# Performance work log

Hardware: AMD Instinct MI355X
Metric: run time of the kernel (lower is better)

The kernel has to match this reference:

```python
import jax, jax.numpy as jnp
import numpy as np

NEG_INF = -1e30
EPS = 1e-6


def _apply_rope_interleaved(x, cos, sin):
    # x: (..., rope_dim); cos/sin broadcastable to (..., rope_dim//2)
    x1 = x[..., 0::2]
    x2 = x[..., 1::2]
    o1 = x1 * cos - x2 * sin
    o2 = x1 * sin + x2 * cos
    return jnp.stack([o1, o2], axis=-1).reshape(x.shape)


def setup_inputs() -> dict:
    key = jax.random.key(0)
    ks = jax.random.split(key, 6)
    B, S, D = 1, 2048, 7168
    H, HD, ROPE, QLR = 64, 128, 64, 1536
    x = jax.random.normal(ks[0], (B, S, D), dtype=jnp.float32)
    q_lora = jax.random.normal(ks[1], (B, S, QLR), dtype=jnp.float32)
    wq_b = jax.random.normal(ks[2], (QLR, H * HD), dtype=jnp.float32) * 0.02
    wk = jax.random.normal(ks[3], (D, HD), dtype=jnp.float32) * 0.02
    weights_proj = jax.random.normal(ks[4], (D, H), dtype=jnp.float32) * 0.02
    k_norm_w = jnp.ones((HD,), dtype=jnp.float32)
    k_norm_b = jnp.zeros((HD,), dtype=jnp.float32)
    # standard RoPE tables for the first ROPE dims
    half = ROPE // 2
    inv_freq = 1.0 / (10000.0 ** (np.arange(half, dtype=np.float64) / half))
    ang = np.arange(S, dtype=np.float64)[:, None] * inv_freq[None, :]
    cos = jnp.asarray(np.cos(ang), dtype=jnp.float32)
    sin = jnp.asarray(np.sin(ang), dtype=jnp.float32)
    return {"x": x, "q_lora": q_lora, "wq_b": wq_b, "wk": wk,
            "weights_proj": weights_proj, "k_norm_w": k_norm_w,
            "k_norm_b": k_norm_b, "cos": cos, "sin": sin, "topk": 512}


def reference(x, q_lora, wq_b, wk, weights_proj, k_norm_w, k_norm_b, cos, sin, topk):
    B, S, D = x.shape
    HD = wk.shape[1]
    H = weights_proj.shape[1]
    ROPE = cos.shape[1] * 2
    # queries: low-rank up-projection -> per-head, RoPE on first ROPE dims
    q = (q_lora @ wq_b).reshape(B, S, H, HD)
    q_pe = _apply_rope_interleaved(q[..., :ROPE], cos[None, :, None, :], sin[None, :, None, :])
    q = jnp.concatenate([q_pe, q[..., ROPE:]], axis=-1)
    # keys: single head, LayerNorm then RoPE on first ROPE dims
    k = x @ wk  # [B,S,HD]
    mu = k.mean(-1, keepdims=True)
    var = ((k - mu) ** 2).mean(-1, keepdims=True)
    k = (k - mu) * jax.lax.rsqrt(var + EPS) * k_norm_w + k_norm_b
    k_pe = _apply_rope_interleaved(k[..., :ROPE], cos[None], sin[None])
    k = jnp.concatenate([k_pe, k[..., ROPE:]], axis=-1)
    # per-token head gates, scaled by n_heads^-0.5 and softmax scale HD^-0.5
    w = (x @ weights_proj) * (H ** -0.5) * (HD ** -0.5)  # [B,S,H]
    # lightning index score: I[t,s] = sum_h w[t,h] * relu(q[t,h] . k[s])
    scores = jax.nn.relu(jnp.einsum('bshd,btd->bsht', q, k))  # [B,S,H,S]
    index_score = jnp.einsum('bsht,bsh->bst', scores, w)      # [B,S,S]
    # causal mask then top-k token selection
    causal = jnp.arange(S)[None, :] <= jnp.arange(S)[:, None]
    index_score = jnp.where(causal[None], index_score, NEG_INF)
    vals, idx = jax.lax.top_k(index_score, topk)
    return vals, idx
```

## Files before the change

### kernel.cpp

```cpp
#include <hip/hip_runtime.h>
#include <stdint.h>

#define S_LEN 2048
#define D_DIM 7168
#define H_NUM 64
#define HD_DIM 128
#define QLR_DIM 1536
#define NQ_DIM 8192
#define ROPE_DIM 64
#define HALF_DIM 32
#define TOPK_N 512
#define NEG_INF_F (-1e30f)
#define LN_EPS 1e-6f
#define W_SCALE 0.011048543456039806f

#define KCHUNKS 7
#define KCHUNK_SZ 1024

#define QF_HSTRIDE (128 * 4 * 64 * 8)

#define QBF_OFF 0
#define ALORA_OFF (QBF_OFF + S_LEN * NQ_DIM / 2)
#define WT_OFF   (ALORA_OFF + S_LEN * QLR_DIM / 2)
#define XBF_OFF  (WT_OFF + NQ_DIM * QLR_DIM / 2)
#define WT2_OFF  (XBF_OFF + S_LEN * D_DIM / 2)
#define KF_OFF   (WT2_OFF + 192 * D_DIM / 2)
#define KBF_OFF  (KF_OFF + S_LEN * HD_DIM)
#define WF_OFF   (KBF_OFF + S_LEN * HD_DIM / 2)
#define SC_OFF   (WF_OFF + S_LEN * H_NUM)

typedef __attribute__((ext_vector_type(8))) short short8;
typedef __attribute__((ext_vector_type(4))) float floatx4;

__device__ __forceinline__ ushort f2bf(float f) {
    unsigned int u = __float_as_uint(f);
    u += 0x7FFFu + ((u >> 16) & 1u);
    return (ushort)(u >> 16);
}
__device__ __forceinline__ unsigned int pack2bf(float lo, float hi) {
    return (unsigned int)f2bf(lo) | ((unsigned int)f2bf(hi) << 16);
}

__device__ __forceinline__ void gld_lds16(const ushort* g, ushort* l) {
    __builtin_amdgcn_global_load_lds(
        (const __attribute__((address_space(1))) unsigned int*)g,
        (__attribute__((address_space(3))) unsigned int*)l, 16, 0, 0);
}

__global__ __launch_bounds__(256) void cast_bf16_kernel(
    const float* __restrict__ in, ushort* __restrict__ out)
{
    int g = (blockIdx.x * 256 + threadIdx.x) * 8;
    float4 a = *(const float4*)&in[g];
    float4 b = *(const float4*)&in[g + 4];
    uint4 v;
    v.x = pack2bf(a.x, a.y); v.y = pack2bf(a.z, a.w);
    v.z = pack2bf(b.x, b.y); v.w = pack2bf(b.z, b.w);
    *(uint4*)&out[g] = v;
}

__global__ __launch_bounds__(256) void transpose_wqb_kernel(
    const float* __restrict__ W, ushort* __restrict__ WT)
{
    __shared__ ushort tl[64][72];
    const int n0 = blockIdx.x * 64, k0 = blockIdx.y * 64;
    const int t = threadIdx.x;
    const int r = t >> 4, c4 = (t & 15) * 4;
#pragma unroll
    for (int u = 0; u < 4; u++) {
        int kk = r + u * 16;
        float4 v = *(const float4*)&W[(size_t)(k0 + kk) * NQ_DIM + n0 + c4];
        tl[c4 + 0][kk] = f2bf(v.x);
        tl[c4 + 1][kk] = f2bf(v.y);
        tl[c4 + 2][kk] = f2bf(v.z);
        tl[c4 + 3][kk] = f2bf(v.w);
    }
    __syncthreads();
#pragma unroll
    for (int u = 0; u < 2; u++) {
        int i = t + u * 256;
        int nr = i >> 3, c8 = (i & 7) * 8;
        uint4 v = *(const uint4*)&tl[nr][c8];
        *(uint4*)&WT[(size_t)(n0 + nr) * QLR_DIM + k0 + c8] = v;
    }
}

__global__ __launch_bounds__(256) void transpose_wkp_kernel(
    const float* __restrict__ WK, const float* __restrict__ WP,
    ushort* __restrict__ WT2)
{
    __shared__ ushort tl[64][72];
    const int ntile = blockIdx.x;
    const int k0 = blockIdx.y * 64;
    const float* src; int ld, cbase;
    if (ntile < 2) { src = WK; ld = HD_DIM; cbase = ntile * 64; }
    else           { src = WP; ld = H_NUM; cbase = 0; }
    const int t = threadIdx.x;
    const int r = t >> 4, c4 = (t & 15) * 4;
#pragma unroll
    for (int u = 0; u < 4; u++) {
        int kk = r + u * 16;
        float4 v = *(const float4*)&src[(size_t)(k0 + kk) * ld + cbase + c4];
        tl[c4 + 0][kk] = f2bf(v.x);
        tl[c4 + 1][kk] = f2bf(v.y);
        tl[c4 + 2][kk] = f2bf(v.z);
        tl[c4 + 3][kk] = f2bf(v.w);
    }
    __syncthreads();
#pragma unroll
    for (int u = 0; u < 2; u++) {
        int i = t + u * 256;
        int nr = i >> 3, c8 = (i & 7) * 8;
        uint4 v = *(const uint4*)&tl[nr][c8];
        *(uint4*)&WT2[(size_t)(ntile * 64 + nr) * D_DIM + k0 + c8] = v;
    }
}

__global__ __launch_bounds__(256) void qgemm_mfma_kernel(
    const ushort* __restrict__ Abf,
    const ushort* __restrict__ WT,
    const float* __restrict__ cosp, const float* __restrict__ sinp,
    ushort* __restrict__ Qo)
{
    __shared__ ushort lds[128 * 136];
    ushort* As = lds;
    ushort* Bs = lds + 8192;

    const int tid = threadIdx.x;
    const int lane = tid & 63;
    const int wave = tid >> 6;
    const int m = lane & 15;
    const int q = lane >> 4;
    const int wm = wave & 1, wn = wave >> 1;
    const int m0 = blockIdx.y * 128;
    const int n0 = blockIdx.x * 128;
    const int h = blockIdx.x;

    floatx4 acc[4][4];
#pragma unroll
    for (int i = 0; i < 4; i++)
#pragma unroll
        for (int j = 0; j < 4; j++) acc[i][j] = (floatx4){0.f, 0.f, 0.f, 0.f};

    const ushort* agp[4];
    const ushort* bgp[4];
    unsigned int sbase[4];
#pragma unroll
    for (int u = 0; u < 4; u++) {
        int s = (u * 4 + wave) * 64 + lane;
        int row = s >> 3, c = s & 7;
        int kg = c ^ (row & 7);
        agp[u] = Abf + (size_t)(m0 + row) * QLR_DIM + kg * 8;
        bgp[u] = WT + (size_t)(n0 + row) * QLR_DIM + kg * 8;
        sbase[u] = (unsigned int)((u * 4 + wave) * 64 * 8);
    }

    for (int kt = 0; kt < QLR_DIM; kt += 64) {
        __syncthreads();
#pragma unroll
        for (int u = 0; u < 4; u++) gld_lds16(agp[u] + kt, &As[sbase[u]]);
#pragma unroll
        for (int u = 0; u < 4; u++) gld_lds16(bgp[u] + kt, &Bs[sbase[u]]);
        __syncthreads();

        short8 af[4][2], bf[4][2];
#pragma unroll
        for (int mt = 0; mt < 4; mt++) {
            int row = wm * 64 + mt * 16 + m;
#pragma unroll
            for (int ks = 0; ks < 2; ks++)
                af[mt][ks] = *(const short8*)
                    &As[row * 64 + ((((ks << 2) + q) ^ (m & 7)) * 8)];
        }
#pragma unroll
        for (int nt = 0; nt < 4; nt++) {
            int row = wn * 64 + nt * 16 + m;
#pragma unroll
            for (int ks = 0; ks < 2; ks++)
                bf[nt][ks] = *(const short8*)
                    &Bs[row * 64 + ((((ks << 2) + q) ^ (m & 7)) * 8)];
        }
#pragma unroll
        for (int mt = 0; mt < 4; mt++)
#pragma unroll
            for (int nt = 0; nt < 4; nt++)
#pragma unroll
                for (int ks = 0; ks < 2; ks++)
                    acc[mt][nt] = __builtin_amdgcn_mfma_f32_16x16x32_bf16(
                        af[mt][ks], bf[nt][ks], acc[mt][nt], 0, 0, 0);
    }

    __syncthreads();
    ushort* ep = lds;

#pragma unroll
    for (int mt = 0; mt < 4; mt++) {
        const int srow_base = m0 + wm * 64 + mt * 16 + q * 4;
#pragma unroll
        for (int nt = 0; nt < 4; nt++) {
            const int d = wn * 64 + nt * 16 + m;
            float o[4];
            if (wn == 0) {
                const int jj = d >> 1;
#pragma unroll
                for (int r = 0; r < 4; r++) {
                    float x = acc[mt][nt][r];
                    float p = __shfl_xor(x, 1, 64);
                    float c = cosp[(srow_base + r) * HALF_DIM + jj];
                    float sn = sinp[(srow_base + r) * HALF_DIM + jj];
                    o[r] = (d & 1) ? (p * sn + x * c) : (x * c - p * sn);
                }
            } else {
#pragma unroll
                for (int r = 0; r < 4; r++) o[r] = acc[mt][nt][r];
            }
#pragma unroll
            for (int r = 0; r < 4; r++)
                ep[(wm * 64 + mt * 16 + q * 4 + r) * 136 + d] = f2bf(o[r]);
        }
    }
    __syncthreads();

    const int sgrp0 = m0 >> 4;
#pragma unroll
    for (int u = 0; u < 8; u++) {
        int i = u * 256 + tid;
        int sgl = i >> 8, c = i & 255;
        int ks = c >> 6, ln = c & 63;
        int srow = sgl * 16 + (ln & 15);
        int d0 = (ks << 5) + ((ln >> 4) << 3);
        uint4 v = *(const uint4*)&ep[srow * 136 + d0];
        size_t dst = (size_t)h * QF_HSTRIDE +
                     ((((size_t)(sgrp0 + sgl) * 4 + ks) * 64 + ln) * 8);
        *(uint4*)&Qo[dst] = v;
    }
}

__global__ __launch_bounds__(256) void kw_mfma_kernel(
    const ushort* __restrict__ Xbf,
    const ushort* __restrict__ WT2,
    float* __restrict__ partial)
{
    __shared__ ushort As[128 * 64];
    __shared__ ushort Bs[64 * 64];

    const int tid = threadIdx.x;
    const int lane = tid & 63;
    const int wave = tid >> 6;
    const int m = lane & 15;
    const int q = lane >> 4;
    const int wm = wave & 1, wn = wave >> 1;
    const int m0 = blockIdx.x * 128;
    const int n0 = blockIdx.y * 64;
    const int kc = blockIdx.z;
    const size_t kbase = (size_t)kc * KCHUNK_SZ;

    const ushort* agp[4];
    unsigned int abase[4];
#pragma unroll
    for (int u = 0; u < 4; u++) {
        int s = (u * 4 + wave) * 64 + lane;
        int row = s >> 3, c = s & 7;
        int kg = c ^ (row & 7);
        agp[u] = Xbf + (size_t)(m0 + row) * D_DIM + kbase + kg * 8;
        abase[u] = (unsigned int)((u * 4 + wave) * 64 * 8);
    }
    const ushort* bgp[2];
    unsigned int bbase[2];
#pragma unroll
    for (int u = 0; u < 2; u++) {
        int s = (u * 4 + wave) * 64 + lane;
        int row = s >> 3, c = s & 7;
        int kg = c ^ (row & 7);
        bgp[u] = WT2 + (size_t)(n0 + row) * D_DIM + kbase + kg * 8;
        bbase[u] = (unsigned int)((u * 4 + wave) * 64 * 8);
    }

    floatx4 acc[4][2];
#pragma unroll
    for (int i = 0; i < 4; i++)
#pragma unroll
        for (int j = 0; j < 2; j++) acc[i][j] = (floatx4){0.f, 0.f, 0.f, 0.f};

    for (int kt = 0; kt < KCHUNK_SZ; kt += 64) {
        __syncthreads();
#pragma unroll
        for (int u = 0; u < 4; u++) gld_lds16(agp[u] + kt, &As[abase[u]]);
#pragma unroll
        for (int u = 0; u < 2; u++) gld_lds16(bgp[u] + kt, &Bs[bbase[u]]);
        __syncthreads();

        short8 af[4][2], bfr[2][2];
#pragma unroll
        for (int mt = 0; mt < 4; mt++) {
            int row = wm * 64 + mt * 16 + m;
#pragma unroll
            for (int ks = 0; ks < 2; ks++)
                af[mt][ks] = *(const short8*)
                    &As[row * 64 + ((((ks << 2) + q) ^ (m & 7)) * 8)];
        }
#pragma unroll
        for (int nt = 0; nt < 2; nt++) {
            int row = wn * 32 + nt * 16 + m;
#pragma unroll
            for (int ks = 0; ks < 2; ks++)
                bfr[nt][ks] = *(const short8*)
                    &Bs[row * 64 + ((((ks << 2) + q) ^ (m & 7)) * 8)];
        }
#pragma unroll
        for (int mt = 0; mt < 4; mt++)
#pragma unroll
            for (int nt = 0; nt < 2; nt++)
#pragma unroll
                for (int ks = 0; ks < 2; ks++)
                    acc[mt][nt] = __builtin_amdgcn_mfma_f32_16x16x32_bf16(
                        af[mt][ks], bfr[nt][ks], acc[mt][nt], 0, 0, 0);
    }

#pragma unroll
    for (int mt = 0; mt < 4; mt++) {
        int grow = m0 + wm * 64 + mt * 16 + q * 4;
#pragma unroll
        for (int nt = 0; nt < 2; nt++) {
            int gn = n0 + wn * 32 + nt * 16 + m;
#pragma unroll
            for (int r = 0; r < 4; r++)
                partial[((size_t)kc * S_LEN + grow + r) * 192 + gn] = acc[mt][nt][r];
        }
    }
}

__global__ __launch_bounds__(256) void kw_reduce_kernel(
    const float* __restrict__ partial, float* __restrict__ Ko, float* __restrict__ Wo)
{
    int g = blockIdx.x * 256 + threadIdx.x;
    int m = g / 192, n = g % 192;
    float s = 0.f;
#pragma unroll
    for (int c = 0; c < KCHUNKS; c++)
        s += partial[((size_t)c * S_LEN + m) * 192 + n];
    if (n < HD_DIM) Ko[(size_t)m * HD_DIM + n] = s;
    else            Wo[(size_t)m * H_NUM + (n - HD_DIM)] = s * W_SCALE;
}

__global__ __launch_bounds__(128) void knorm_rope_kernel(
    const float* __restrict__ Kf, const float* __restrict__ gw, const float* __restrict__ gb,
    const float* __restrict__ cosp, const float* __restrict__ sinp,
    ushort* __restrict__ Kbf)
{
    __shared__ float red[128];
    __shared__ float sh[128];
    const int m = blockIdx.x, t = threadIdx.x;
    float v = Kf[(size_t)m * HD_DIM + t];
    red[t] = v; __syncthreads();
    for (int off = 64; off > 0; off >>= 1) {
        if (t < off) red[t] += red[t + off];
        __syncthreads();
    }
    float mu = red[0] * (1.f / HD_DIM);
    __syncthreads();
    float dv = v - mu;
    red[t] = dv * dv; __syncthreads();
    for (int off = 64; off > 0; off >>= 1) {
        if (t < off) red[t] += red[t + off];
        __syncthreads();
    }
    float var = red[0] * (1.f / HD_DIM);
    float rs = rsqrtf(var + LN_EPS);
    float kn = dv * rs * gw[t] + gb[t];
    sh[t] = kn; __syncthreads();
    float out;
    if (t < ROPE_DIM) {
        int jj = t >> 1;
        float c = cosp[m * HALF_DIM + jj], sn = sinp[m * HALF_DIM + jj];
        out = ((t & 1) == 0) ? (sh[t] * c - sh[t + 1] * sn)
                             : (sh[t - 1] * sn + sh[t] * c);
    } else {
        out = kn;
    }
    Kbf[(size_t)m * HD_DIM + t] = f2bf(out);
}

__global__ __launch_bounds__(256, 2) void attn_mfma_kernel(
    const ushort* __restrict__ Qb,
    const ushort* __restrict__ Kb,
    const float* __restrict__ Wf,
    float* __restrict__ SC)
{
    __shared__ float Wsm[64 * 68];

    const int bidx = blockIdx.x;
    const int x = bidx & 7, j = bidx >> 3;
    const int g1 = x + 1, g2 = 32 - x, g3 = x + 9;
    int ts, tt;
    if (j < g1)                { ts = x;      tt = j; }
    else if (j < g1 + g2)      { ts = 31 - x; tt = j - g1; }
    else if (j < g1 + g2 + g3) { ts = x + 8;  tt = j - g1 - g2; }
    else                       { ts = 23 - x; tt = j - g1 - g2 - g3; }
    const int s0 = ts * 64, t0 = tt * 64;

    const int tid = threadIdx.x;
    const int lane = tid & 63;
    const int m = lane & 15;
    const int q = lane >> 4;
    const int strip = (tid >> 6) * 16;

    {
        const float4* gw = (const float4*)(Wf + (size_t)s0 * H_NUM);
#pragma unroll
        for (int u = 0; u < 4; u++) {
            int ch = tid + u * 256;
            float4 v = gw[ch];
            *(float4*)&Wsm[(ch >> 4) * 68 + (ch & 15) * 4] = v;
        }
    }

    short8 bf[4][4];
#pragma unroll
    for (int tile = 0; tile < 4; tile++)
#pragma unroll
        for (int ks = 0; ks < 4; ks++)
            bf[tile][ks] = *(const short8*)
                &Kb[(size_t)(t0 + tile * 16 + m) * HD_DIM + ks * 32 + q * 8];

    __syncthreads();

    float acc[4][4];
#pragma unroll
    for (int tile = 0; tile < 4; tile++)
#pragma unroll
        for (int r = 0; r < 4; r++) acc[tile][r] = 0.f;

    const int sgrp = ts * 4 + (strip >> 4);
    const ushort* qfb = Qb + ((size_t)sgrp * 4 * 64 + lane) * 8;
    const float* wrow = &Wsm[(strip + q * 4) * 68];

    auto loadQ = [&](short8* dst, int h) {
        const ushort* p = qfb + (size_t)h * QF_HSTRIDE;
#pragma unroll
        for (int ks = 0; ks < 4; ks++) dst[ks] = *(const short8*)&p[ks * 512];
    };
    auto computeH = [&](const short8* af, int h) {
        float wv[4];
#pragma unroll
        for (int r = 0; r < 4; r++) wv[r] = wrow[r * 68 + h];
#pragma unroll
        for (int tile = 0; tile < 4; tile++) {
            floatx4 p = {0.f, 0.f, 0.f, 0.f};
#pragma unroll
            for (int ks = 0; ks < 4; ks++)
                p = __builtin_amdgcn_mfma_f32_16x16x32_bf16(af[ks], bf[tile][ks], p, 0, 0, 0);
#pragma unroll
            for (int r = 0; r < 4; r++)
                acc[tile][r] += fmaxf(p[r], 0.f) * wv[r];
        }
    };

    short8 afA[4], afB[4];
    loadQ(afA, 0);
    for (int h = 0; h < H_NUM; h += 2) {
        loadQ(afB, h + 1);
        computeH(afA, h);
        if (h + 2 < H_NUM) loadQ(afA, h + 2);
        computeH(afB, h + 1);
    }

#pragma unroll
    for (int tile = 0; tile < 4; tile++)
#pragma unroll
        for (int r = 0; r < 4; r++)
            SC[(size_t)(s0 + strip + q * 4 + r) * S_LEN + t0 + tile * 16 + m] =
                acc[tile][r];
}

__device__ __forceinline__ unsigned int fkey(float f) {
    unsigned int u = __float_as_uint(f);
    return (u & 0x80000000u) ? ~u : (u | 0x80000000u);
}

__global__ __launch_bounds__(256) void topk_kernel(
    const float* __restrict__ SC, float* __restrict__ outv, float* __restrict__ outi)
{
    __shared__ unsigned int key[S_LEN];
    __shared__ float val[S_LEN];
    const int s = blockIdx.x, tid = threadIdx.x;
    const int nchunks = (s >> 9) + 1;
    const int nact = nchunks << 9;

    for (int t = tid; t < nact; t += 256) {
        float v = (t <= s) ? SC[(size_t)s * S_LEN + t] : NEG_INF_F;
        val[t] = v;
        key[t] = (fkey(v) & 0xFFFFF800u) | (unsigned int)(S_LEN - 1 - t);
    }
    __syncthreads();

    for (int k2 = 2; k2 <= 512; k2 <<= 1) {
        for (int j = k2 >> 1; j > 0; j >>= 1) {
            for (int p = tid; p < (nact >> 1); p += 256) {
                int i = 2 * p - (p & (j - 1));
                int il = i & 511;
                unsigned int a = key[i], b = key[i + j];
                bool up = ((il & k2) == 0);
                bool sw = up ? (a < b) : (a > b);
                if (sw) { key[i] = b; key[i + j] = a; }
            }
            __syncthreads();
        }
    }

    for (int c = 1; c < nchunks; c++) {
        for (int p = tid; p < 512; p += 256) {
            unsigned int a = key[p], b = key[(c << 9) + 511 - p];
            key[p] = a > b ? a : b;
        }
        __syncthreads();
        for (int j = 256; j > 0; j >>= 1) {
            int p = tid;
            int i = 2 * p - (p & (j - 1));
            unsigned int a = key[i], b = key[i + j];
            if (a < b) { key[i] = b; key[i + j] = a; }
            __syncthreads();
        }
    }

    for (int i2 = tid; i2 < TOPK_N; i2 += 256) {
        unsigned int kv = key[i2];
        int t = S_LEN - 1 - (int)(kv & 0x7FFu);
        outv[(size_t)s * TOPK_N + i2] = val[t];
        outi[(size_t)s * TOPK_N + i2] = (float)t;
    }
}

extern "C" void kernel_launch(void* const* d_in, const int* in_sizes, int n_in,
                              void* d_out, int out_size, void* d_ws, size_t ws_size,
                              hipStream_t stream)
{
    (void)in_sizes; (void)n_in; (void)out_size; (void)ws_size;
    const float* x      = (const float*)d_in[0];
    const float* q_lora = (const float*)d_in[1];
    const float* wq_b   = (const float*)d_in[2];
    const float* wk     = (const float*)d_in[3];
    const float* wproj  = (const float*)d_in[4];
    const float* knw    = (const float*)d_in[5];
    const float* knb    = (const float*)d_in[6];
    const float* cosp   = (const float*)d_in[7];
    const float* sinp   = (const float*)d_in[8];

    float* ws = (float*)d_ws;
    ushort* Qbf  = (ushort*)(ws + QBF_OFF);
    ushort* Albf = (ushort*)(ws + ALORA_OFF);
    ushort* WTbf = (ushort*)(ws + WT_OFF);
    ushort* Xbf  = (ushort*)(ws + XBF_OFF);
    ushort* WT2  = (ushort*)(ws + WT2_OFF);
    float*  Kf   = ws + KF_OFF;
    ushort* Kbf  = (ushort*)(ws + KBF_OFF);
    float*  Wf   = ws + WF_OFF;
    float*  SCb  = ws + SC_OFF;
    float*  partial = ws + SC_OFF;

    float* outv = (float*)d_out;
    float* outi = outv + (size_t)S_LEN * TOPK_N;

    cast_bf16_kernel<<<(S_LEN * QLR_DIM) / (256 * 8), 256, 0, stream>>>(q_lora, Albf);
    cast_bf16_kernel<<<(S_LEN * D_DIM) / (256 * 8), 256, 0, stream>>>(x, Xbf);
    transpose_wqb_kernel<<<dim3(NQ_DIM / 64, QLR_DIM / 64), 256, 0, stream>>>(wq_b, WTbf);
    transpose_wkp_kernel<<<dim3(3, D_DIM / 64), 256, 0, stream>>>(wk, wproj, WT2);
    kw_mfma_kernel<<<dim3(S_LEN / 128, 3, KCHUNKS), 256, 0, stream>>>(Xbf, WT2, partial);
    kw_reduce_kernel<<<(S_LEN * 192) / 256, 256, 0, stream>>>(partial, Kf, Wf);
    knorm_rope_kernel<<<S_LEN, 128, 0, stream>>>(Kf, knw, knb, cosp, sinp, Kbf);
    qgemm_mfma_kernel<<<dim3(NQ_DIM / 128, S_LEN / 128), 256, 0, stream>>>(
        Albf, WTbf, cosp, sinp, Qbf);
    attn_mfma_kernel<<<528, 256, 0, stream>>>(Qbf, Kbf, Wf, SCb);
    topk_kernel<<<S_LEN, 256, 0, stream>>>(SCb, outv, outi);
}
```

Measured before the change: 347.0 us.

## Rewrite Q GEMM as 256x256 tile double-buffered pipeline with XCD-aware block mapping

The Q up-projection GEMM moves from 128x128 tiles with 4 waves and single-buffered LDS to 256x256 tiles with 8 waves. The K loop is double-buffered, with global-to-LDS loads for the next stage issued between four MFMA sub-phases, plus explicit waitcnt, barriers and setprio around the MFMA bursts. Blocks are remapped so neighbouring tiles share an XCD, which aims to improve L2 reuse. The goal is to hide load latency and raise arithmetic intensity, at the cost of 128KB LDS per block, which limits occupancy, and a more fragile hand-tuned schedule.

Measured after the change: 340.7 us. Within noise of the previous version (-1.8%).

```diff
diff --git a/kernel.cpp b/kernel.cpp
--- a/kernel.cpp
+++ b/kernel.cpp
@@ -16,6 +16,7 @@
 
 #define KCHUNKS 7
 #define KCHUNK_SZ 1024
+#define NKT 24
 
 #define QF_HSTRIDE (128 * 4 * 64 * 8)
 
@@ -116,123 +117,217 @@
     }
 }
 
-__global__ __launch_bounds__(256) void qgemm_mfma_kernel(
+__global__ __launch_bounds__(512, 2) void qgemm_mfma_kernel(
     const ushort* __restrict__ Abf,
     const ushort* __restrict__ WT,
     const float* __restrict__ cosp, const float* __restrict__ sinp,
     ushort* __restrict__ Qo)
 {
-    __shared__ ushort lds[128 * 136];
-    ushort* As = lds;
-    ushort* Bs = lds + 8192;
+    __shared__ __align__(16) ushort lds[65536];
 
     const int tid = threadIdx.x;
     const int lane = tid & 63;
     const int wave = tid >> 6;
     const int m = lane & 15;
     const int q = lane >> 4;
-    const int wm = wave & 1, wn = wave >> 1;
-    const int m0 = blockIdx.y * 128;
-    const int n0 = blockIdx.x * 128;
-    const int h = blockIdx.x;
-
-    floatx4 acc[4][4];
-#pragma unroll
-    for (int i = 0; i < 4; i++)
+    const int wm = wave & 1;
+    const int wn = wave >> 1;
+
+    const int wg = blockIdx.x;
+    const int xcd = wg & 7, lid = wg >> 3;
+    const int bx = xcd * 4 + (lid & 3);
+    const int by = lid >> 2;
+    const int m0 = by * 256;
+    const int n0 = bx * 256;
+
+    const ushort* sgA[2][2];
+    const ushort* sgB[2][2];
+    unsigned int ldoff[2][2];
+#pragma unroll
+    for (int h = 0; h < 2; h++)
+#pragma unroll
+        for (int r = 0; r < 2; r++) {
+            int s = r * 512 + wave * 64 + lane;
+            int row = s >> 3, c = s & 7;
+            int kg = c ^ (row & 7);
+            sgA[h][r] = Abf + (size_t)(m0 + h * 128 + row) * QLR_DIM + kg * 8;
+            sgB[h][r] = WT  + (size_t)(n0 + h * 128 + row) * QLR_DIM + kg * 8;
+            ldoff[h][r] = (unsigned int)(h * 8192 + (r * 512 + wave * 64) * 8);
+        }
+
+    auto stageA = [&](int kt, int h) {
+        ushort* dbase = &lds[(kt & 1) * 16384];
+        gld_lds16(sgA[h][0] + kt * 64, dbase + ldoff[h][0]);
+        gld_lds16(sgA[h][1] + kt * 64, dbase + ldoff[h][1]);
+    };
+    auto stageB = [&](int kt, int h) {
+        ushort* dbase = &lds[32768 + (kt & 1) * 16384];
+        gld_lds16(sgB[h][0] + kt * 64, dbase + ldoff[h][0]);
+        gld_lds16(sgB[h][1] + kt * 64, dbase + ldoff[h][1]);
+    };
+
+    unsigned int aoff[2], boff[2];
+#pragma unroll
+    for (int ks = 0; ks < 2; ks++) {
+        unsigned int xr = (unsigned int)(((((ks << 2) + q) ^ (m & 7))) * 8);
+        aoff[ks] = (unsigned int)((wm * 128 + m) * 64) + xr;
+        boff[ks] = (unsigned int)((wn * 64 + m) * 64) + xr;
+    }
+
+    floatx4 acc[8][4];
+#pragma unroll
+    for (int i = 0; i < 8; i++)
 #pragma unroll
         for (int j = 0; j < 4; j++) acc[i][j] = (floatx4){0.f, 0.f, 0.f, 0.f};
 
-    const ushort* agp[4];
-    const ushort* bgp[4];
-    unsigned int sbase[4];
-#pragma unroll
-    for (int u = 0; u < 4; u++) {
-        int s = (u * 4 + wave) * 64 + lane;
-        int row = s >> 3, c = s & 7;
-        int kg = c ^ (row & 7);
-        agp[u] = Abf + (size_t)(m0 + row) * QLR_DIM + kg * 8;
-        bgp[u] = WT + (size_t)(n0 + row) * QLR_DIM + kg * 8;
-        sbase[u] = (unsigned int)((u * 4 + wave) * 64 * 8);
-    }
-
-    for (int kt = 0; kt < QLR_DIM; kt += 64) {
-        __syncthreads();
-#pragma unroll
-        for (int u = 0; u < 4; u++) gld_lds16(agp[u] + kt, &As[sbase[u]]);
-#pragma unroll
-        for (int u = 0; u < 4; u++) gld_lds16(bgp[u] + kt, &Bs[sbase[u]]);
-        __syncthreads();
-
-        short8 af[4][2], bf[4][2];
-#pragma unroll
-        for (int mt = 0; mt < 4; mt++) {
-            int row = wm * 64 + mt * 16 + m;
+    stageA(0, 0); stageA(0, 1); stageB(0, 0); stageB(0, 1);
+    stageA(1, 0); stageA(1, 1);
+    asm volatile("s_waitcnt vmcnt(4)" ::: "memory");
+    __builtin_amdgcn_s_barrier();
+
+    short8 af[4][2], bfr[2][2];
+
+    for (int kt = 0; kt < NKT; ++kt) {
+        const ushort* as = &lds[(kt & 1) * 16384];
+        const ushort* bs = &lds[32768 + (kt & 1) * 16384];
+
+#pragma unroll
+        for (int mt = 0; mt < 4; mt++)
 #pragma unroll
             for (int ks = 0; ks < 2; ks++)
-                af[mt][ks] = *(const short8*)
-                    &As[row * 64 + ((((ks << 2) + q) ^ (m & 7)) * 8)];
-        }
-#pragma unroll
-        for (int nt = 0; nt < 4; nt++) {
-            int row = wn * 64 + nt * 16 + m;
+                af[mt][ks] = *(const short8*)&as[aoff[ks] + mt * 1024];
+#pragma unroll
+        for (int nt = 0; nt < 2; nt++)
 #pragma unroll
             for (int ks = 0; ks < 2; ks++)
-                bf[nt][ks] = *(const short8*)
-                    &Bs[row * 64 + ((((ks << 2) + q) ^ (m & 7)) * 8)];
-        }
+                bfr[nt][ks] = *(const short8*)&bs[boff[ks] + nt * 1024];
+        if (kt + 1 < NKT) stageB(kt + 1, 0);
+        __builtin_amdgcn_s_barrier();
+        asm volatile("s_waitcnt lgkmcnt(0)" ::: "memory");
+        __builtin_amdgcn_s_setprio(1);
 #pragma unroll
         for (int mt = 0; mt < 4; mt++)
 #pragma unroll
-            for (int nt = 0; nt < 4; nt++)
+            for (int nt = 0; nt < 2; nt++)
 #pragma unroll
                 for (int ks = 0; ks < 2; ks++)
                     acc[mt][nt] = __builtin_amdgcn_mfma_f32_16x16x32_bf16(
-                        af[mt][ks], bf[nt][ks], acc[mt][nt], 0, 0, 0);
+                        af[mt][ks], bfr[nt][ks], acc[mt][nt], 0, 0, 0);
+        __builtin_amdgcn_s_setprio(0);
+        __builtin_amdgcn_s_barrier();
+
+#pragma unroll
+        for (int nt = 0; nt < 2; nt++)
+#pragma unroll
+            for (int ks = 0; ks < 2; ks++)
+                bfr[nt][ks] = *(const short8*)&bs[boff[ks] + 2048 + nt * 1024];
+        if (kt + 1 < NKT) stageB(kt + 1, 1);
+        __builtin_amdgcn_s_barrier();
+        asm volatile("s_waitcnt lgkmcnt(0)" ::: "memory");
+        __builtin_amdgcn_s_setprio(1);
+#pragma unroll
+        for (int mt = 0; mt < 4; mt++)
+#pragma unroll
+            for (int nt = 0; nt < 2; nt++)
+#pragma unroll
+                for (int ks = 0; ks < 2; ks++)
+                    acc[mt][2 + nt] = __builtin_amdgcn_mfma_f32_16x16x32_bf16(
+                        af[mt][ks], bfr[nt][ks], acc[mt][2 + nt], 0, 0, 0);
+        __builtin_amdgcn_s_setprio(0);
+        __builtin_amdgcn_s_barrier();
+
+#pragma unroll
+        for (int mt = 0; mt < 4; mt++)
+#pragma unroll
+            for (int ks = 0; ks < 2; ks++)
+                af[mt][ks] = *(const short8*)&as[aoff[ks] + 4096 + mt * 1024];
+        __builtin_amdgcn_s_barrier();
+        asm volatile("s_waitcnt lgkmcnt(0)" ::: "memory");
+        __builtin_amdgcn_s_setprio(1);
+#pragma unroll
+        for (int mt = 0; mt < 4; mt++)
+#pragma unroll
+            for (int nt = 0; nt < 2; nt++)
+#pragma unroll
+                for (int ks = 0; ks < 2; ks++)
+                    acc[4 + mt][2 + nt] = __builtin_amdgcn_mfma_f32_16x16x32_bf16(
+                        af[mt][ks], bfr[nt][ks], acc[4 + mt][2 + nt], 0, 0, 0);
+        __builtin_amdgcn_s_setprio(0);
+        __builtin_amdgcn_s_barrier();
+
+#pragma unroll
+        for (int nt = 0; nt < 2; nt++)
+#pragma unroll
+            for (int ks = 0; ks < 2; ks++)
+                bfr[nt][ks] = *(const short8*)&bs[boff[ks] + nt * 1024];
+        if (kt + 2 < NKT) { stageA(kt + 2, 0); stageA(kt + 2, 1); }
+        __builtin_amdgcn_s_barrier();
+        asm volatile("s_waitcnt lgkmcnt(0)" ::: "memory");
+        __builtin_amdgcn_s_setprio(1);
+#pragma unroll
+        for (int mt = 0; mt < 4; mt++)
+#pragma unroll
+            for (int nt = 0; nt < 2; nt++)
+#pragma unroll
+                for (int ks = 0; ks < 2; ks++)
+                    acc[4 + mt][nt] = __builtin_amdgcn_mfma_f32_16x16x32_bf16(
+                        af[mt][ks], bfr[nt][ks], acc[4 + mt][nt], 0, 0, 0);
+        __builtin_amdgcn_s_setprio(0);
+        if (kt >= NKT - 2) asm volatile("s_waitcnt vmcnt(0)" ::: "memory");
+        else               asm volatile("s_waitcnt vmcnt(4)" ::: "memory");
+        __builtin_amdgcn_s_barrier();
     }
 
     __syncthreads();
     ushort* ep = lds;
-
-#pragma unroll
-    for (int mt = 0; mt < 4; mt++) {
-        const int srow_base = m0 + wm * 64 + mt * 16 + q * 4;
-#pragma unroll
-        for (int nt = 0; nt < 4; nt++) {
-            const int d = wn * 64 + nt * 16 + m;
-            float o[4];
-            if (wn == 0) {
-                const int jj = d >> 1;
-#pragma unroll
-                for (int r = 0; r < 4; r++) {
-                    float x = acc[mt][nt][r];
-                    float p = __shfl_xor(x, 1, 64);
-                    float c = cosp[(srow_base + r) * HALF_DIM + jj];
-                    float sn = sinp[(srow_base + r) * HALF_DIM + jj];
-                    o[r] = (d & 1) ? (p * sn + x * c) : (x * c - p * sn);
+    const int h0 = bx * 2;
+    const int sgrp0 = m0 >> 4;
+
+#pragma unroll
+    for (int hh = 0; hh < 2; hh++) {
+        if ((wn >> 1) == hh) {
+            const int dbase = (wn & 1) * 64;
+            const bool do_rope = ((wn & 1) == 0);
+#pragma unroll
+            for (int ai = 0; ai < 8; ai++) {
+                const int srow0 = m0 + wm * 128 + ai * 16 + q * 4;
+#pragma unroll
+                for (int bj = 0; bj < 4; bj++) {
+                    const int d = dbase + bj * 16 + m;
+                    float o[4];
+                    if (do_rope) {
+                        const int jj = d >> 1;
+#pragma unroll
+                        for (int r = 0; r < 4; r++) {
+                            float x = acc[ai][bj][r];
+                            float p = __shfl_xor(x, 1, 64);
+                            float c = cosp[(srow0 + r) * HALF_DIM + jj];
+                            float sn = sinp[(srow0 + r) * HALF_DIM + jj];
+                            o[r] = (d & 1) ? (p * sn + x * c) : (x * c - p * sn);
+                        }
+                    } else {
+#pragma unroll
+                        for (int r = 0; r < 4; r++) o[r] = acc[ai][bj][r];
+                    }
+#pragma unroll
+                    for (int r = 0; r < 4; r++)
+                        ep[(wm * 128 + ai * 16 + q * 4 + r) * 136 + d] = f2bf(o[r]);
                 }
-            } else {
-#pragma unroll
-                for (int r = 0; r < 4; r++) o[r] = acc[mt][nt][r];
             }
-#pragma unroll
-            for (int r = 0; r < 4; r++)
-                ep[(wm * 64 + mt * 16 + q * 4 + r) * 136 + d] = f2bf(o[r]);
-        }
-    }
-    __syncthreads();
-
-    const int sgrp0 = m0 >> 4;
-#pragma unroll
-    for (int u = 0; u < 8; u++) {
-        int i = u * 256 + tid;
-        int sgl = i >> 8, c = i & 255;
-        int ks = c >> 6, ln = c & 63;
-        int srow = sgl * 16 + (ln & 15);
-        int d0 = (ks << 5) + ((ln >> 4) << 3);
-        uint4 v = *(const uint4*)&ep[srow * 136 + d0];
-        size_t dst = (size_t)h * QF_HSTRIDE +
-                     ((((size_t)(sgrp0 + sgl) * 4 + ks) * 64 + ln) * 8);
-        *(uint4*)&Qo[dst] = v;
+        }
+        __syncthreads();
+        const size_t hstr = (size_t)(h0 + hh) * QF_HSTRIDE;
+#pragma unroll
+        for (int u = 0; u < 8; u++) {
+            int i = u * 512 + tid;
+            int sgl = i >> 8, c = i & 255;
+            int ks = c >> 6, ln = c & 63;
+            int srow = sgl * 16 + (ln & 15);
+            int d0 = (ks << 5) + ((ln >> 4) << 3);
+            uint4 v = *(const uint4*)&ep[srow * 136 + d0];
+            *(uint4*)&Qo[hstr + ((((size_t)(sgrp0 + sgl) * 4 + ks) * 64 + ln) * 8)] = v;
+        }
+        __syncthreads();
     }
 }
 
@@ -568,8 +663,7 @@
     kw_mfma_kernel<<<dim3(S_LEN / 128, 3, KCHUNKS), 256, 0, stream>>>(Xbf, WT2, partial);
     kw_reduce_kernel<<<(S_LEN * 192) / 256, 256, 0, stream>>>(partial, Kf, Wf);
     knorm_rope_kernel<<<S_LEN, 128, 0, stream>>>(Kf, knw, knb, cosp, sinp, Kbf);
-    qgemm_mfma_kernel<<<dim3(NQ_DIM / 128, S_LEN / 128), 256, 0, stream>>>(
-        Albf, WTbf, cosp, sinp, Qbf);
+    qgemm_mfma_kernel<<<256, 512, 0, stream>>>(Albf, WTbf, cosp, sinp, Qbf);
     attn_mfma_kernel<<<528, 256, 0, stream>>>(Qbf, Kbf, Wf, SCb);
     topk_kernel<<<S_LEN, 256, 0, stream>>>(SCb, outv, outi);
 }
```
